# Kernel optimization log

Hardware: AMD Instinct MI355X
Metric: run time of the kernel (lower is better)

Reference implementation:

```python
import jax, jax.numpy as jnp
import numpy as np

GAMMA = 0.5
EPS = 1e-06
REL_THRESH = 1e-09


def setup_inputs() -> dict:
    key = jax.random.key(0)
    k1, k2 = jax.random.split(key)
    B, T, D = 4, 4096, 256
    A_rel = jax.random.uniform(k1, (B, T, T), dtype=jnp.float32)
    # symmetrize as the docstring states A_rel is symmetric
    A_rel = 0.5 * (A_rel + jnp.swapaxes(A_rel, -1, -2))
    k_seq = jax.random.normal(k2, (B, T, D), dtype=jnp.float32)
    return {"A_rel": A_rel, "k_seq": k_seq}


def reference(A_rel, k_seq):
    # init_sequence: symmetric normalization W = D^{-1/2} A D^{-1/2}
    D = jnp.sum(A_rel, axis=-1) + EPS                  # (B, T)
    d_inv_sqrt = 1.0 / jnp.sqrt(D)                     # (B, T)
    W = A_rel * d_inv_sqrt[:, :, None] * d_inv_sqrt[:, None, :]  # (B, T, T)

    T = A_rel.shape[1]
    # step t uses W[:, t, :t+1] -> lower-triangular (incl. diagonal) causal mask
    tril = jnp.tril(jnp.ones((T, T), dtype=W.dtype))   # (T, T)
    W_causal = W * tril                                # (B, T, T)

    # a_t = sum_{s<=t} W[b,t,s] * k_s  for every t at once
    a = jnp.einsum('bts,bsd->btd', W_causal, k_seq)    # (B, T, D)

    # has_relation[b,t] = max_{s<=t} |W[b,t,s]| > 1e-9
    has_relation = jnp.max(jnp.abs(W) * tril, axis=-1) > REL_THRESH  # (B, T)

    a_scaled = a * jnp.sqrt(jnp.asarray(GAMMA, dtype=a.dtype))
    out = a_scaled * has_relation[:, :, None].astype(a_scaled.dtype)
    return out
```

## Files before the change

### kernel.cpp

```cpp
#include <hip/hip_runtime.h>
#include <hip/hip_bf16.h>

constexpr int Bn = 4;
constexpr int Tn = 4096;
constexpr int Dn = 256;
constexpr int NT = Tn / 64;
constexpr int NTRI = NT * (NT + 1) / 2;

using ushort = unsigned short;
typedef short short8 __attribute__((ext_vector_type(8)));
typedef float f32x4 __attribute__((ext_vector_type(4)));

__device__ __forceinline__ ushort f2bu(float f) {
    __hip_bfloat16 h = __float2bfloat16(f);
    return __builtin_bit_cast(unsigned short, h);
}
__device__ __forceinline__ void gld_lds16(const ushort* g, ushort* l) {
    __builtin_amdgcn_global_load_lds((const __attribute__((address_space(1))) void*)g,
                                     (__attribute__((address_space(3))) void*)l,
                                     16, 0, 0);
}
__device__ __forceinline__ float dis_of(float a) { return rsqrtf(a + 1e-6f); }

__global__ __launch_bounds__(256) void tri_pass_kernel(
    const float* __restrict__ A, float* __restrict__ acc, ushort* __restrict__ Apk) {
    __shared__ float tile[64][68];
    int bid = blockIdx.x;
    int b = bid / NTRI;
    int r = bid - b * NTRI;
    int it = (int)((sqrtf(8.f * r + 1.f) - 1.f) * 0.5f);
    while ((it + 1) * (it + 2) / 2 <= r) ++it;
    while (it * (it + 1) / 2 > r) --it;
    int kt = r - it * (it + 1) / 2;
    int t0 = it * 64, s0 = kt * 64;
    bool diag = (kt == it);

    int tid = threadIdx.x;
    int i = tid >> 2;
    int c0 = (tid & 3) * 16;

    const float* g = A + ((size_t)(b * Tn + t0 + i) * Tn + s0 + c0);
    float4 v[4];
#pragma unroll
    for (int q = 0; q < 4; ++q) v[q] = *(const float4*)(g + 4 * q);

    float f[16];
#pragma unroll
    for (int q = 0; q < 4; ++q) {
        f[4 * q + 0] = v[q].x; f[4 * q + 1] = v[q].y;
        f[4 * q + 2] = v[q].z; f[4 * q + 3] = v[q].w;
    }
    float rp = 0.f;
#pragma unroll
    for (int e = 0; e < 16; ++e) rp += f[e];
    rp += __shfl_xor(rp, 1, 64);
    rp += __shfl_xor(rp, 2, 64);
    if ((tid & 3) == 0) atomicAdd(&acc[b * Tn + t0 + i], rp);

#pragma unroll
    for (int q = 0; q < 4; ++q) *(float4*)&tile[i][c0 + 4 * q] = v[q];

    ushort* tb = Apk + (size_t)b * NTRI * 4096 + (size_t)(it * (it + 1) / 2 + kt) * 4096;
    unsigned w[8];
#pragma unroll
    for (int e = 0; e < 8; ++e) {
        float lo = f[2 * e], hi = f[2 * e + 1];
        if (diag) {
            if (c0 + 2 * e > i)     lo = 0.f;
            if (c0 + 2 * e + 1 > i) hi = 0.f;
        }
        w[e] = (unsigned)f2bu(lo) | ((unsigned)f2bu(hi) << 16);
    }
    *(uint4*)(tb + i * 64 + c0)     = make_uint4(w[0], w[1], w[2], w[3]);
    *(uint4*)(tb + i * 64 + c0 + 8) = make_uint4(w[4], w[5], w[6], w[7]);

    if (!diag) {
        __syncthreads();
        int j = tid & 63, p = tid >> 6;
        float cp = 0.f;
#pragma unroll
        for (int q = 0; q < 16; ++q) cp += tile[p * 16 + q][j];
        atomicAdd(&acc[b * Tn + s0 + j], cp);
    }
}

__global__ __launch_bounds__(256) void scale_transpose_kernel(
    const float* __restrict__ K, const float* __restrict__ acc, ushort* __restrict__ kT) {
    int bid = blockIdx.x;
    int b = bid >> 8;
    int rr = bid & 255;
    int st = rr >> 2, dt = rr & 3;
    int s0 = st * 64, d0 = dt * 64;
    __shared__ ushort tile[64][72];
    int tid = threadIdx.x;
#pragma unroll
    for (int q = 0; q < 2; ++q) {
        int idx = q * 256 + tid;
        int sl = idx >> 3, dl0 = (idx & 7) * 8;
        const float* g = K + ((size_t)(b * Tn + s0 + sl) * Dn + d0 + dl0);
        float sc = dis_of(acc[b * Tn + s0 + sl]);
        float4 v0 = *(const float4*)g;
        float4 v1 = *(const float4*)(g + 4);
        tile[sl][dl0 + 0] = f2bu(v0.x * sc);
        tile[sl][dl0 + 1] = f2bu(v0.y * sc);
        tile[sl][dl0 + 2] = f2bu(v0.z * sc);
        tile[sl][dl0 + 3] = f2bu(v0.w * sc);
        tile[sl][dl0 + 4] = f2bu(v1.x * sc);
        tile[sl][dl0 + 5] = f2bu(v1.y * sc);
        tile[sl][dl0 + 6] = f2bu(v1.z * sc);
        tile[sl][dl0 + 7] = f2bu(v1.w * sc);
    }
    __syncthreads();
#pragma unroll
    for (int q = 0; q < 2; ++q) {
        int idx = q * 256 + tid;
        int dl = idx >> 3, sl0 = (idx & 7) * 8;
        unsigned w[4];
#pragma unroll
        for (int e = 0; e < 4; ++e) {
            unsigned lo = tile[sl0 + 2 * e][dl];
            unsigned hi = tile[sl0 + 2 * e + 1][dl];
            w[e] = lo | (hi << 16);
        }
        *(uint4*)(kT + ((size_t)(b * Dn + d0 + dl) * Tn + s0 + sl0)) =
            make_uint4(w[0], w[1], w[2], w[3]);
    }
}

constexpr int BK = 64;

__global__ __launch_bounds__(256) void gemm_causal_kernel(
    const ushort* __restrict__ Apk, const ushort* __restrict__ kT,
    const float* __restrict__ acc_in, float* __restrict__ out) {
    __shared__ __attribute__((aligned(16))) ushort As[2][64 * BK];
    __shared__ __attribute__((aligned(16))) ushort Bs[2][64 * BK];
    __shared__ float rs[64];

    int bid = blockIdx.x;
    int it = 63 - (bid >> 4);
    int sub = bid & 15;
    int b = sub >> 2;
    int d0 = (sub & 3) * 64;
    int t0 = it * 64;

    int tid = threadIdx.x;
    int lane = tid & 63;
    int w = tid >> 6;
    int l15 = lane & 15;
    int kq = (lane >> 4) * 8;

    const ushort* Atri = Apk + (size_t)b * NTRI * 4096 + (size_t)(it * (it + 1) / 2) * 4096;
    const size_t kTbase = (size_t)(b * Dn + d0) * Tn;

    if (tid < 64) rs[tid] = 0.70710678118654752f * dis_of(acc_in[b * Tn + t0 + tid]);

    f32x4 acc[2][2];
#pragma unroll
    for (int mi = 0; mi < 2; ++mi)
#pragma unroll
        for (int ni = 0; ni < 2; ++ni) acc[mi][ni] = (f32x4){0.f, 0.f, 0.f, 0.f};

    int mrow = (w >> 1) * 32;
    int ncol = (w & 1) * 32;
    int nkt = it + 1;

    auto stage = [&](int buf, int kt) {
#pragma unroll
        for (int q = 0; q < 2; ++q) {
            int idx = q * 256 + tid;
            gld_lds16(Atri + (size_t)kt * 4096 + idx * 8, &As[buf][idx * 8]);
        }
#pragma unroll
        for (int q = 0; q < 2; ++q) {
            int idx = q * 256 + tid;
            int n = idx >> 3, sc = (idx & 7) * 8;
            gld_lds16(kT + kTbase + (size_t)n * Tn + kt * BK + sc, &Bs[buf][idx * 8]);
        }
    };

    stage(0, 0);
    __syncthreads();

    for (int kt = 0; kt < nkt; ++kt) {
        int cur = kt & 1;
        if (kt + 1 < nkt) stage(cur ^ 1, kt + 1);
#pragma unroll
        for (int ki = 0; ki < 2; ++ki) {
            int kc = ki * 32 + kq;
            short8 af[2];
#pragma unroll
            for (int mi = 0; mi < 2; ++mi)
                af[mi] = *(const short8*)&As[cur][(mrow + 16 * mi + l15) * BK + kc];
            short8 bfr[2];
#pragma unroll
            for (int ni = 0; ni < 2; ++ni)
                bfr[ni] = *(const short8*)&Bs[cur][(ncol + 16 * ni + l15) * BK + kc];
#pragma unroll
            for (int mi = 0; mi < 2; ++mi)
#pragma unroll
                for (int ni = 0; ni < 2; ++ni)
                    acc[mi][ni] = __builtin_amdgcn_mfma_f32_16x16x32_bf16(
                        af[mi], bfr[ni], acc[mi][ni], 0, 0, 0);
        }
        __syncthreads();
    }

#pragma unroll
    for (int mi = 0; mi < 2; ++mi) {
#pragma unroll
        for (int ni = 0; ni < 2; ++ni) {
            int tl = mrow + 16 * mi + (lane >> 4) * 4;
            int d = d0 + ncol + 16 * ni + l15;
#pragma unroll
            for (int r = 0; r < 4; ++r) {
                int t = t0 + tl + r;
                out[(size_t)(b * Tn + t) * Dn + d] = acc[mi][ni][r] * rs[tl + r];
            }
        }
    }
}

extern "C" void kernel_launch(void* const* d_in, const int* in_sizes, int n_in,
                              void* d_out, int out_size, void* d_ws, size_t ws_size,
                              hipStream_t stream) {
    const float* A = (const float*)d_in[0];
    const float* K = (const float*)d_in[1];
    float* out = (float*)d_out;

    float* acc = (float*)d_ws;
    ushort* kT = (ushort*)(acc + Bn * Tn);
    ushort* Apk = kT + (size_t)Bn * Dn * Tn;

    hipMemsetAsync(acc, 0, Bn * Tn * sizeof(float), stream);
    tri_pass_kernel<<<dim3(Bn * NTRI), dim3(256), 0, stream>>>(A, acc, Apk);
    scale_transpose_kernel<<<dim3(Bn * (Tn / 64) * (Dn / 64)), dim3(256), 0, stream>>>(K, acc, kT);
    gemm_causal_kernel<<<dim3(NT * 16), dim3(256), 0, stream>>>(Apk, kT, acc, out);
}
```

Before: 400.3 us.

## Pair row tiles in causal GEMM with swizzled LDS and nontemporal A loads

After: 403.0 us. About the same (+0.7%).

```diff
diff --git a/kernel.cpp b/kernel.cpp
--- a/kernel.cpp
+++ b/kernel.cpp
@@ -10,6 +10,7 @@
 using ushort = unsigned short;
 typedef short short8 __attribute__((ext_vector_type(8)));
 typedef float f32x4 __attribute__((ext_vector_type(4)));
+typedef float f32x4v __attribute__((ext_vector_type(4)));
 
 __device__ __forceinline__ ushort f2bu(float f) {
     __hip_bfloat16 h = __float2bfloat16(f);
@@ -40,15 +41,15 @@
     int c0 = (tid & 3) * 16;
 
     const float* g = A + ((size_t)(b * Tn + t0 + i) * Tn + s0 + c0);
-    float4 v[4];
-#pragma unroll
-    for (int q = 0; q < 4; ++q) v[q] = *(const float4*)(g + 4 * q);
+    f32x4v v[4];
+#pragma unroll
+    for (int q = 0; q < 4; ++q) v[q] = __builtin_nontemporal_load((const f32x4v*)(g + 4 * q));
 
     float f[16];
 #pragma unroll
     for (int q = 0; q < 4; ++q) {
-        f[4 * q + 0] = v[q].x; f[4 * q + 1] = v[q].y;
-        f[4 * q + 2] = v[q].z; f[4 * q + 3] = v[q].w;
+        f[4 * q + 0] = v[q][0]; f[4 * q + 1] = v[q][1];
+        f[4 * q + 2] = v[q][2]; f[4 * q + 3] = v[q][3];
     }
     float rp = 0.f;
 #pragma unroll
@@ -58,7 +59,7 @@
     if ((tid & 3) == 0) atomicAdd(&acc[b * Tn + t0 + i], rp);
 
 #pragma unroll
-    for (int q = 0; q < 4; ++q) *(float4*)&tile[i][c0 + 4 * q] = v[q];
+    for (int q = 0; q < 4; ++q) *(f32x4v*)&tile[i][c0 + 4 * q] = v[q];
 
     ushort* tb = Apk + (size_t)b * NTRI * 4096 + (size_t)(it * (it + 1) / 2 + kt) * 4096;
     unsigned w[8];
@@ -127,54 +128,64 @@
     }
 }
 
-constexpr int BK = 64;
-
 __global__ __launch_bounds__(256) void gemm_causal_kernel(
     const ushort* __restrict__ Apk, const ushort* __restrict__ kT,
-    const float* __restrict__ acc_in, float* __restrict__ out) {
-    __shared__ __attribute__((aligned(16))) ushort As[2][64 * BK];
-    __shared__ __attribute__((aligned(16))) ushort Bs[2][64 * BK];
-    __shared__ float rs[64];
+    const float* __restrict__ acc_in, float* __restrict__ out,
+    const ushort* __restrict__ zsrc) {
+    __shared__ __attribute__((aligned(16))) ushort As[2][128 * 64];
+    __shared__ __attribute__((aligned(16))) ushort Bs[2][64 * 64];
+    __shared__ float rs[128];
 
     int bid = blockIdx.x;
-    int it = 63 - (bid >> 4);
+    int g = bid >> 4;
     int sub = bid & 15;
+    int it2 = (g < 16) ? (31 - g) : (g - 16);
     int b = sub >> 2;
     int d0 = (sub & 3) * 64;
-    int t0 = it * 64;
+    int itA = 2 * it2, itB = 2 * it2 + 1;
+    int t0 = itA * 64;
+    int nkt = 2 * it2 + 2;
 
     int tid = threadIdx.x;
     int lane = tid & 63;
     int w = tid >> 6;
     int l15 = lane & 15;
-    int kq = (lane >> 4) * 8;
-
-    const ushort* Atri = Apk + (size_t)b * NTRI * 4096 + (size_t)(it * (it + 1) / 2) * 4096;
+
+    const ushort* ApkA = Apk + (size_t)b * NTRI * 4096 + (size_t)(itA * (itA + 1) / 2) * 4096;
+    const ushort* ApkB = Apk + (size_t)b * NTRI * 4096 + (size_t)(itB * (itB + 1) / 2) * 4096;
     const size_t kTbase = (size_t)(b * Dn + d0) * Tn;
 
-    if (tid < 64) rs[tid] = 0.70710678118654752f * dis_of(acc_in[b * Tn + t0 + tid]);
-
-    f32x4 acc[2][2];
-#pragma unroll
-    for (int mi = 0; mi < 2; ++mi)
+    if (tid < 128) rs[tid] = 0.70710678118654752f * dis_of(acc_in[b * Tn + t0 + tid]);
+
+    f32x4 acc[4][2];
+#pragma unroll
+    for (int mi = 0; mi < 4; ++mi)
 #pragma unroll
         for (int ni = 0; ni < 2; ++ni) acc[mi][ni] = (f32x4){0.f, 0.f, 0.f, 0.f};
 
-    int mrow = (w >> 1) * 32;
+    int mrow = (w >> 1) * 64;
     int ncol = (w & 1) * 32;
-    int nkt = it + 1;
 
     auto stage = [&](int buf, int kt) {
+        bool lastA = (kt == itB);
+        const ushort* baseA = ApkA + (size_t)kt * 4096;
+        const ushort* baseB = ApkB + (size_t)kt * 4096;
+#pragma unroll
+        for (int q = 0; q < 4; ++q) {
+            int idx = q * 256 + tid;
+            int row = idx >> 3, ch = idx & 7;
+            int sch = ((ch ^ (row & 7)) << 3);
+            const ushort* src;
+            if (row < 64) src = lastA ? zsrc : (baseA + row * 64 + sch);
+            else          src = baseB + (size_t)(row - 64) * 64 + sch;
+            gld_lds16(src, &As[buf][idx * 8]);
+        }
 #pragma unroll
         for (int q = 0; q < 2; ++q) {
             int idx = q * 256 + tid;
-            gld_lds16(Atri + (size_t)kt * 4096 + idx * 8, &As[buf][idx * 8]);
-        }
-#pragma unroll
-        for (int q = 0; q < 2; ++q) {
-            int idx = q * 256 + tid;
-            int n = idx >> 3, sc = (idx & 7) * 8;
-            gld_lds16(kT + kTbase + (size_t)n * Tn + kt * BK + sc, &Bs[buf][idx * 8]);
+            int n = idx >> 3, ch = idx & 7;
+            int sch = ((ch ^ (n & 7)) << 3);
+            gld_lds16(kT + kTbase + (size_t)n * Tn + kt * 64 + sch, &Bs[buf][idx * 8]);
         }
     };
 
@@ -186,17 +197,21 @@
         if (kt + 1 < nkt) stage(cur ^ 1, kt + 1);
 #pragma unroll
         for (int ki = 0; ki < 2; ++ki) {
-            int kc = ki * 32 + kq;
-            short8 af[2];
-#pragma unroll
-            for (int mi = 0; mi < 2; ++mi)
-                af[mi] = *(const short8*)&As[cur][(mrow + 16 * mi + l15) * BK + kc];
+            int kch = ki * 4 + (lane >> 4);
+            short8 af[4];
+#pragma unroll
+            for (int mi = 0; mi < 4; ++mi) {
+                int rrow = mrow + 16 * mi + l15;
+                af[mi] = *(const short8*)&As[cur][rrow * 64 + ((kch ^ (rrow & 7)) << 3)];
+            }
             short8 bfr[2];
 #pragma unroll
-            for (int ni = 0; ni < 2; ++ni)
-                bfr[ni] = *(const short8*)&Bs[cur][(ncol + 16 * ni + l15) * BK + kc];
-#pragma unroll
-            for (int mi = 0; mi < 2; ++mi)
+            for (int ni = 0; ni < 2; ++ni) {
+                int n = ncol + 16 * ni + l15;
+                bfr[ni] = *(const short8*)&Bs[cur][n * 64 + ((kch ^ (n & 7)) << 3)];
+            }
+#pragma unroll
+            for (int mi = 0; mi < 4; ++mi)
 #pragma unroll
                 for (int ni = 0; ni < 2; ++ni)
                     acc[mi][ni] = __builtin_amdgcn_mfma_f32_16x16x32_bf16(
@@ -206,7 +221,7 @@
     }
 
 #pragma unroll
-    for (int mi = 0; mi < 2; ++mi) {
+    for (int mi = 0; mi < 4; ++mi) {
 #pragma unroll
         for (int ni = 0; ni < 2; ++ni) {
             int tl = mrow + 16 * mi + (lane >> 4) * 4;
@@ -230,9 +245,11 @@
     float* acc = (float*)d_ws;
     ushort* kT = (ushort*)(acc + Bn * Tn);
     ushort* Apk = kT + (size_t)Bn * Dn * Tn;
+    ushort* zsrc = Apk + (size_t)Bn * NTRI * 4096;
 
     hipMemsetAsync(acc, 0, Bn * Tn * sizeof(float), stream);
+    hipMemsetAsync(zsrc, 0, 256, stream);
     tri_pass_kernel<<<dim3(Bn * NTRI), dim3(256), 0, stream>>>(A, acc, Apk);
     scale_transpose_kernel<<<dim3(Bn * (Tn / 64) * (Dn / 64)), dim3(256), 0, stream>>>(K, acc, kT);
-    gemm_causal_kernel<<<dim3(NT * 16), dim3(256), 0, stream>>>(Apk, kT, acc, out);
-}
+    gemm_causal_kernel<<<dim3(512), dim3(256), 0, stream>>>(Apk, kT, acc, out, zsrc);
+}
```
